# Performance work log

Measured on AMD Instinct MI355X. Metric: run time of the kernel, lower is better.

The kernel has to match this reference:

```python
import jax, jax.numpy as jnp
import numpy as np

B, T, N, F = 4, 24, 1024, 128
EPS = 1e-5  # torch nn.LayerNorm default
FRONT_T = 12  # hard-coded graph_array[:12] split in the original module
MIN_NUMBER = 3  # hard-coded topk k


def setup_inputs() -> dict:
    key = jax.random.key(0)
    ks = jax.random.split(key, 7)
    sc = 0.05
    return {
        "input": jax.random.normal(ks[0], (B, T, N, F), jnp.float32),
        # torch nn.Linear stores weight as [out, in]; y = x @ W.T + b
        "W_xff": jax.random.normal(ks[1], (3 * F, F), jnp.float32) * sc,
        "b_xff": jax.random.normal(ks[2], (3 * F,), jnp.float32) * sc,
        "W_ff1": jax.random.normal(ks[3], (F, F), jnp.float32) * sc,
        "b_ff1": jnp.zeros((F,), jnp.float32),
        "W_ff2": jax.random.normal(ks[4], (F, F), jnp.float32) * sc,
        "b_ff2": jnp.zeros((F,), jnp.float32),
        "ln_g": jnp.ones((F,), jnp.float32),
        "ln_b": jnp.zeros((F,), jnp.float32),
    }


def _mixup_last(front, y):
    # front: [12, N, F]; y: scalar int (data-dependent column index).
    # mixup_region with block_size=1: replace column y with the mean of
    # columns [max(y-1,0), min(y+2,N)), cast through uint8 (as original).
    n = front.shape[1]
    y_start = jnp.maximum(y - 1, 0)
    y_end = jnp.minimum(y + 2, n)
    cols = jnp.arange(n)
    mask = ((cols >= y_start) & (cols < y_end)).astype(front.dtype)  # [N]
    cnt = (y_end - y_start).astype(front.dtype)
    mixed = (front * mask[None, :, None]).sum(axis=1) / cnt  # [12, F]
    # .to(torch.uint8) truncates and kills gradient for this column
    mixed = jax.lax.stop_gradient(mixed.astype(jnp.uint8).astype(front.dtype))
    return front.at[:, y, :].set(mixed)


def reference(input, W_xff, b_xff, W_ff1, b_ff1, W_ff2, b_ff2, ln_g, ln_b):
    f = input.shape[-1]
    x_ = input @ W_xff.T + b_xff  # [B,T,N,3F]
    q, k, v = x_[..., :f], x_[..., f:2 * f], x_[..., 2 * f:]
    e = jnp.einsum('btnf,btmf->btnm', q, k) / jnp.sqrt(jnp.asarray(f, x_.dtype))
    attn = jax.nn.softmax(e, axis=-1)  # [B,T,N,N]

    # detached attention maps drive the topk row selection
    attn_d = jax.lax.stop_gradient(attn)
    col_sums = attn_d.sum(axis=2)  # torch sum(dim=1) per [T,N,N] -> [B,T,N]
    # torch.topk(largest=False, sorted=True): 3 smallest, ascending by value
    _, idx = jax.lax.top_k(-col_sums, MIN_NUMBER)  # [B,T,3]
    # NOTE: the original loop reassigns `graph_array = mixup_region(graph_array_front, ...)`
    # each iteration, so only the LAST mixup (i = T-1, 3rd smallest index) survives.
    y_last = idx[:, -1, -1]  # [B]

    front = v[:, :FRONT_T]   # [B,12,N,F]
    back = v[:, FRONT_T:]    # [B,T-12,N,F]
    new_front = jax.vmap(_mixup_last)(front, y_last)
    new_value = jnp.concatenate([new_front, back], axis=1)  # [B,T,N,F]

    value_i = jnp.einsum('btnm,btmf->btnf', attn, new_value)
    h = jax.nn.gelu(value_i @ W_ff1.T + b_ff1, approximate=False) @ W_ff2.T + b_ff2
    res = h + input
    mu = res.mean(-1, keepdims=True)
    var = ((res - mu) ** 2).mean(-1, keepdims=True)
    return (res - mu) / jnp.sqrt(var + EPS) * ln_g + ln_b
```

## Files before the change

kernel.cpp:

```cpp
#include <hip/hip_runtime.h>
#include <math.h>

#define BB 4
#define TT 24
#define BN 1024
#define FD 128
#define BT (BB*TT)
#define BTN (BT*BN)
#define FRONT_T 12
#define SCALE 0.08838834764831845f
#define GELU_K 0.7071067811865476f

typedef __attribute__((ext_vector_type(8))) short s8v;
typedef __attribute__((ext_vector_type(4))) float f4v;

static __device__ __forceinline__ unsigned short f2bf(float f) {
    union { float f; unsigned u; } c; c.f = f;
    unsigned u = c.u + 0x7FFFu + ((c.u >> 16) & 1u);
    return (unsigned short)(u >> 16);
}

__global__ __launch_bounds__(256) void k_convx(const float* __restrict__ x,
                                               unsigned short* __restrict__ xb) {
    size_t i = ((size_t)blockIdx.x * 256 + threadIdx.x) * 4;
    float4 v = *(const float4*)(x + i);
    ushort4 h = {f2bf(v.x), f2bf(v.y), f2bf(v.z), f2bf(v.w)};
    *(ushort4*)(xb + i) = h;
}

__global__ void k_convw(const float* __restrict__ W, unsigned short* __restrict__ wb, int n) {
    int i = blockIdx.x * 256 + threadIdx.x;
    if (i < n) wb[i] = f2bf(W[i]);
}

__global__ __launch_bounds__(256, 2) void k_qkv_mfma(
    const unsigned short* __restrict__ xb, const unsigned short* __restrict__ wb,
    const float* __restrict__ bias,
    unsigned short* __restrict__ qb16, unsigned short* __restrict__ kb16,
    unsigned short* __restrict__ vtb)
{
    __shared__ __attribute__((aligned(16))) unsigned short Xs[64 * 136];
    __shared__ __attribute__((aligned(16))) unsigned short Ws[64 * 136];
    __shared__ __attribute__((aligned(16))) unsigned short Cs[64 * 72];
    const int tid = threadIdx.x;
    const int rowBase = blockIdx.x * 64;
    const int colBase = blockIdx.y * 64;
    const int lane = tid & 63, wave = tid >> 6;
    const int lx = lane & 15, quad = lane >> 4;

    for (int i = 0; i < 4; ++i) {
        int idx = i * 256 + tid, r = idx >> 4, c8 = idx & 15;
        *(int4*)(&Xs[r * 136 + c8 * 8]) = *(const int4*)(xb + (size_t)(rowBase + r) * FD + c8 * 8);
    }
    for (int i = 0; i < 4; ++i) {
        int idx = i * 256 + tid, r = idx >> 4, c8 = idx & 15;
        *(int4*)(&Ws[r * 136 + c8 * 8]) = *(const int4*)(wb + (size_t)(colBase + r) * FD + c8 * 8);
    }
    __syncthreads();

    f4v acc[4];
    for (int gg = 0; gg < 4; ++gg) acc[gg] = (f4v){0.f, 0.f, 0.f, 0.f};
    for (int t4 = 0; t4 < 4; ++t4) {
        s8v a = *(const s8v*)(&Xs[(wave * 16 + lx) * 136 + t4 * 32 + quad * 8]);
        for (int gg = 0; gg < 4; ++gg) {
            s8v b = *(const s8v*)(&Ws[(gg * 16 + lx) * 136 + t4 * 32 + quad * 8]);
            acc[gg] = __builtin_amdgcn_mfma_f32_16x16x32_bf16(a, b, acc[gg], 0, 0, 0);
        }
    }

    const int n0 = wave * 16 + quad * 4;
    if (colBase < 2 * FD) {
        for (int gg = 0; gg < 4; ++gg) {
            float bb = bias[colBase + gg * 16 + lx];
            for (int r = 0; r < 4; ++r)
                Cs[(n0 + r) * 72 + gg * 16 + lx] = f2bf(acc[gg][r] + bb);
        }
        __syncthreads();
        unsigned short* dst = (colBase < FD) ? qb16 : kb16;
        const int cc0 = colBase & (FD - 1);
        for (int i = 0; i < 2; ++i) {
            int idx = i * 256 + tid, r = idx >> 3, c8 = idx & 7;
            *(int4*)(dst + (size_t)(rowBase + r) * FD + cc0 + c8 * 8) =
                *(const int4*)(&Cs[r * 72 + c8 * 8]);
        }
    } else {
        for (int gg = 0; gg < 4; ++gg) {
            float bb = bias[colBase + gg * 16 + lx];
            for (int r = 0; r < 4; ++r)
                Cs[(gg * 16 + lx) * 72 + n0 + r] = f2bf(acc[gg][r] + bb);
        }
        __syncthreads();
        const int bt = rowBase >> 10, nBase = rowBase & 1023, cc0 = colBase - 2 * FD;
        for (int i = 0; i < 2; ++i) {
            int idx = i * 256 + tid, f = idx >> 3, c8 = idx & 7;
            *(int4*)(vtb + ((size_t)bt * FD + cc0 + f) * BN + nBase + c8 * 8) =
                *(const int4*)(&Cs[f * 72 + c8 * 8]);
        }
    }
}

__global__ __launch_bounds__(256) void k_qkv32(const float* __restrict__ x,
                                               const float* __restrict__ W,
                                               const float* __restrict__ bias,
                                               float* __restrict__ q32c,
                                               float* __restrict__ k32c) {
    __shared__ float Xs[32][129];
    __shared__ float Ws[64][129];
    const int tid = threadIdx.x;
    const int b = blockIdx.x >> 5;
    const int rt = blockIdx.x & 31;
    const int xrow0 = (b * TT + (TT - 1)) * BN + rt * 32;
    const int colBase = blockIdx.y * 64;

    for (int i = 0; i < 4; ++i) {
        int idx = i * 256 + tid;
        int r = idx >> 5, c4 = idx & 31;
        *(float4*)(&Xs[r][c4 * 4]) = *(const float4*)(x + (size_t)(xrow0 + r) * FD + c4 * 4);
    }
    for (int i = 0; i < 8; ++i) {
        int idx = i * 256 + tid;
        int r = idx >> 5, c4 = idx & 31;
        *(float4*)(&Ws[r][c4 * 4]) = *(const float4*)(W + (size_t)(colBase + r) * FD + c4 * 4);
    }
    __syncthreads();

    const int tx = tid & 15, ty = tid >> 4;
    const int r0 = ty * 2, r1 = ty * 2 + 1;
    float acc0[4] = {0.f, 0.f, 0.f, 0.f};
    float acc1[4] = {0.f, 0.f, 0.f, 0.f};
    for (int kk = 0; kk < FD; ++kk) {
        float a0 = Xs[r0][kk], a1 = Xs[r1][kk];
        float b0 = Ws[tx * 4 + 0][kk];
        float b1 = Ws[tx * 4 + 1][kk];
        float b2 = Ws[tx * 4 + 2][kk];
        float b3 = Ws[tx * 4 + 3][kk];
        acc0[0] += a0 * b0; acc0[1] += a0 * b1; acc0[2] += a0 * b2; acc0[3] += a0 * b3;
        acc1[0] += a1 * b0; acc1[1] += a1 * b1; acc1[2] += a1 * b2; acc1[3] += a1 * b3;
    }
    const int c = colBase + tx * 4;
    float4 bia = *(const float4*)(bias + c);
    float* dst = (c < FD) ? q32c : k32c;
    int cc = (c < FD) ? c : c - FD;
    size_t base = ((size_t)b * BN + rt * 32 + r0) * FD + cc;
    *(float4*)(dst + base)      = make_float4(acc0[0] + bia.x, acc0[1] + bia.y, acc0[2] + bia.z, acc0[3] + bia.w);
    *(float4*)(dst + base + FD) = make_float4(acc1[0] + bia.x, acc1[1] + bia.y, acc1[2] + bia.z, acc1[3] + bia.w);
}

__global__ __launch_bounds__(256) void k_pass1(const float* __restrict__ q32c,
                                               const float* __restrict__ k32c,
                                               float* __restrict__ Mp,
                                               float* __restrict__ Lp) {
    __shared__ float Qs[32][129];
    __shared__ float Ks[64][129];
    const int tid = threadIdx.x;
    const int chunk = blockIdx.y;
    const int b = blockIdx.z;
    const int rowBase = blockIdx.x * 32;
    const float* qb = q32c + (size_t)b * BN * FD;
    const float* kb = k32c + (size_t)b * BN * FD;

    for (int i = 0; i < 4; ++i) {
        int idx = i * 256 + tid;
        int r = idx >> 5, c4 = idx & 31;
        *(float4*)(&Qs[r][c4 * 4]) = *(const float4*)(qb + (size_t)(rowBase + r) * FD + c4 * 4);
    }
    const int tx = tid & 15, ty = tid >> 4;
    const int r0 = ty * 2, r1 = ty * 2 + 1;
    float m[2] = {-1e30f, -1e30f};
    float l[2] = {0.f, 0.f};

    for (int ct = chunk * 4; ct < chunk * 4 + 4; ++ct) {
        __syncthreads();
        for (int i = 0; i < 8; ++i) {
            int idx = i * 256 + tid;
            int r = idx >> 5, c4 = idx & 31;
            *(float4*)(&Ks[r][c4 * 4]) = *(const float4*)(kb + (size_t)(ct * 64 + r) * FD + c4 * 4);
        }
        __syncthreads();
        float e0[4] = {0.f, 0.f, 0.f, 0.f};
        float e1[4] = {0.f, 0.f, 0.f, 0.f};
        for (int kk = 0; kk < FD; ++kk) {
            float a0 = Qs[r0][kk], a1 = Qs[r1][kk];
            float b0 = Ks[tx * 4 + 0][kk];
            float b1 = Ks[tx * 4 + 1][kk];
            float b2 = Ks[tx * 4 + 2][kk];
            float b3 = Ks[tx * 4 + 3][kk];
            e0[0] += a0 * b0; e0[1] += a0 * b1; e0[2] += a0 * b2; e0[3] += a0 * b3;
            e1[0] += a1 * b0; e1[1] += a1 * b1; e1[2] += a1 * b2; e1[3] += a1 * b3;
        }
        float* ep[2] = {e0, e1};
        for (int rr = 0; rr < 2; ++rr) {
            float s0 = ep[rr][0] * SCALE, s1 = ep[rr][1] * SCALE;
            float s2 = ep[rr][2] * SCALE, s3 = ep[rr][3] * SCALE;
            float tm = fmaxf(fmaxf(s0, s1), fmaxf(s2, s3));
            for (int s = 1; s < 16; s <<= 1) tm = fmaxf(tm, __shfl_xor(tm, s, 64));
            float ts = __expf(s0 - tm) + __expf(s1 - tm) + __expf(s2 - tm) + __expf(s3 - tm);
            for (int s = 1; s < 16; s <<= 1) ts += __shfl_xor(ts, s, 64);
            float mn = fmaxf(m[rr], tm);
            l[rr] = l[rr] * __expf(m[rr] - mn) + ts * __expf(tm - mn);
            m[rr] = mn;
        }
    }
    if (tx == 0) {
        size_t base = (size_t)chunk * BB * BN + (size_t)b * BN + rowBase;
        Mp[base + r0] = m[0];
        Lp[base + r0] = l[0];
        Mp[base + r1] = m[1];
        Lp[base + r1] = l[1];
    }
}

__global__ void k_mergeML(const float* __restrict__ Mp, const float* __restrict__ Lp,
                          float* __restrict__ Mv, float* __restrict__ Lv) {
    int i = blockIdx.x * 256 + threadIdx.x;
    if (i >= BB * BN) return;
    float m = -1e30f, l = 0.f;
    for (int c = 0; c < 4; ++c) {
        float mc = Mp[(size_t)c * BB * BN + i];
        float lc = Lp[(size_t)c * BB * BN + i];
        float mn = fmaxf(m, mc);
        l = l * __expf(m - mn) + lc * __expf(mc - mn);
        m = mn;
    }
    Mv[i] = m;
    Lv[i] = l;
}

__global__ __launch_bounds__(256) void k_colsum(const float* __restrict__ q32c,
                                                const float* __restrict__ k32c,
                                                const float* __restrict__ Mv,
                                                const float* __restrict__ Lv,
                                                float* __restrict__ csp) {
    __shared__ float Qs[32][129];
    __shared__ float Ks[64][129];
    __shared__ float red[16][68];
    const int tid = threadIdx.x;
    const int rchunk = blockIdx.y;
    const int b = blockIdx.z;
    const int colBase = blockIdx.x * 64;
    const float* qb = q32c + (size_t)b * BN * FD;
    const float* kb = k32c + (size_t)b * BN * FD;
    const int tx = tid & 15, ty = tid >> 4;
    const int r0 = ty * 2, r1 = ty * 2 + 1;

    for (int i = 0; i < 8; ++i) {
        int idx = i * 256 + tid;
        int r = idx >> 5, c4 = idx & 31;
        *(float4*)(&Ks[r][c4 * 4]) = *(const float4*)(kb + (size_t)(colBase + r) * FD + c4 * 4);
    }

    float acc[4] = {0.f, 0.f, 0.f, 0.f};
    for (int rt = rchunk * 4; rt < rchunk * 4 + 4; ++rt) {
        __syncthreads();
        for (int i = 0; i < 4; ++i) {
            int idx = i * 256 + tid;
            int r = idx >> 5, c4 = idx & 31;
            *(float4*)(&Qs[r][c4 * 4]) = *(const float4*)(qb + (size_t)(rt * 32 + r) * FD + c4 * 4);
        }
        __syncthreads();
        float e0[4] = {0.f, 0.f, 0.f, 0.f};
        float e1[4] = {0.f, 0.f, 0.f, 0.f};
        for (int kk = 0; kk < FD; ++kk) {
            float a0 = Qs[r0][kk], a1 = Qs[r1][kk];
            float b0 = Ks[tx * 4 + 0][kk];
            float b1 = Ks[tx * 4 + 1][kk];
            float b2 = Ks[tx * 4 + 2][kk];
            float b3 = Ks[tx * 4 + 3][kk];
            e0[0] += a0 * b0; e0[1] += a0 * b1; e0[2] += a0 * b2; e0[3] += a0 * b3;
            e1[0] += a1 * b0; e1[1] += a1 * b1; e1[2] += a1 * b2; e1[3] += a1 * b3;
        }
        int n0 = rt * 32 + r0, n1 = rt * 32 + r1;
        float m0 = Mv[(size_t)b * BN + n0], il0 = 1.0f / Lv[(size_t)b * BN + n0];
        float m1 = Mv[(size_t)b * BN + n1], il1 = 1.0f / Lv[(size_t)b * BN + n1];
        for (int j = 0; j < 4; ++j) {
            acc[j] += __expf(e0[j] * SCALE - m0) * il0;
            acc[j] += __expf(e1[j] * SCALE - m1) * il1;
        }
    }
    for (int j = 0; j < 4; ++j) red[ty][tx * 4 + j] = acc[j];
    __syncthreads();
    if (tid < 64) {
        float s = 0.f;
        for (int i = 0; i < 16; ++i) s += red[i][tid];
        csp[((size_t)rchunk * BB + b) * BN + colBase + tid] = s;
    }
}

__global__ void k_top3(const float* __restrict__ csp, int* __restrict__ ylast) {
    __shared__ float sv[192];
    __shared__ int si[192];
    const int b = blockIdx.x;
    const int t = threadIdx.x;
    float bv[3] = {1e30f, 1e30f, 1e30f};
    int bi[3] = {0x7fffffff, 0x7fffffff, 0x7fffffff};
    for (int i = 0; i < 16; ++i) {
        int idx = t * 16 + i;
        float vv = 0.f;
        for (int c = 0; c < 8; ++c)
            vv += csp[((size_t)c * BB + b) * BN + idx];
        if (vv < bv[0]) {
            bv[2] = bv[1]; bi[2] = bi[1];
            bv[1] = bv[0]; bi[1] = bi[0];
            bv[0] = vv;    bi[0] = idx;
        } else if (vv < bv[1]) {
            bv[2] = bv[1]; bi[2] = bi[1];
            bv[1] = vv;    bi[1] = idx;
        } else if (vv < bv[2]) {
            bv[2] = vv;    bi[2] = idx;
        }
    }
    for (int j = 0; j < 3; ++j) { sv[t * 3 + j] = bv[j]; si[t * 3 + j] = bi[j]; }
    __syncthreads();
    if (t == 0) {
        float fv[3] = {1e30f, 1e30f, 1e30f};
        int fi[3] = {0x7fffffff, 0x7fffffff, 0x7fffffff};
        for (int c = 0; c < 192; ++c) {
            float vv = sv[c]; int ii = si[c];
            if (vv < fv[0] || (vv == fv[0] && ii < fi[0])) {
                fv[2] = fv[1]; fi[2] = fi[1];
                fv[1] = fv[0]; fi[1] = fi[0];
                fv[0] = vv;    fi[0] = ii;
            } else if (vv < fv[1] || (vv == fv[1] && ii < fi[1])) {
                fv[2] = fv[1]; fi[2] = fi[1];
                fv[1] = vv;    fi[1] = ii;
            } else if (vv < fv[2] || (vv == fv[2] && ii < fi[2])) {
                fv[2] = vv;    fi[2] = ii;
            }
        }
        ylast[b] = fi[2];
    }
}

__global__ void k_mixup(const float* __restrict__ x, const float* __restrict__ W,
                        const float* __restrict__ bias,
                        unsigned short* __restrict__ vtb,
                        const int* __restrict__ ylast) {
    const int b = blockIdx.y, t = blockIdx.x, f = threadIdx.x;
    const int y = ylast[b];
    const int ys = max(y - 1, 0), ye = min(y + 2, BN);
    const float* wrow = W + (size_t)(2 * FD + f) * FD;
    const float bia = bias[2 * FD + f];
    float s = 0.f;
    for (int r = ys; r < ye; ++r) {
        const float* xrow = x + ((size_t)(b * TT + t) * BN + r) * FD;
        float acc = 0.f;
        for (int kk = 0; kk < FD; ++kk) acc += xrow[kk] * wrow[kk];
        s += acc + bia;
    }
    s /= (float)(ye - ys);
    int ti = (int)s;
    unsigned u = ((unsigned)ti) & 0xFFu;
    vtb[((size_t)(b * TT + t) * FD + f) * BN + y] = f2bf((float)u);
}

__global__ __launch_bounds__(256, 2) void k_flash(
    const unsigned short* __restrict__ qb, const unsigned short* __restrict__ kb,
    const unsigned short* __restrict__ vtb, float* __restrict__ vi)
{
    __shared__ __attribute__((aligned(16))) unsigned short Qs[64 * 136];
    __shared__ __attribute__((aligned(16))) unsigned short Ks[64 * 136];
    __shared__ __attribute__((aligned(16))) unsigned short Vts[128 * 72];
    __shared__ __attribute__((aligned(16))) unsigned short Ps[4][16 * 72];
    const int tid = threadIdx.x;
    const int bt = blockIdx.y;
    const int rowBase = blockIdx.x * 64;
    const int lane = tid & 63, wave = tid >> 6;
    const int lx = lane & 15, quad = lane >> 4;

    const unsigned short* qg = qb + ((size_t)bt * BN + rowBase) * FD;
    for (int i = 0; i < 4; ++i) {
        int idx = i * 256 + tid, r = idx >> 4, c8 = idx & 15;
        *(int4*)(&Qs[r * 136 + c8 * 8]) = *(const int4*)(qg + r * FD + c8 * 8);
    }
    __syncthreads();

    s8v aq[4];
    for (int t4 = 0; t4 < 4; ++t4)
        aq[t4] = *(const s8v*)(&Qs[(wave * 16 + lx) * 136 + t4 * 32 + quad * 8]);

    f4v O[8];
    for (int gg = 0; gg < 8; ++gg) O[gg] = (f4v){0.f, 0.f, 0.f, 0.f};
    float mrow[4] = {-1e30f, -1e30f, -1e30f, -1e30f};
    float lrow[4] = {0.f, 0.f, 0.f, 0.f};

    const unsigned short* kgbase = kb + (size_t)bt * BN * FD;
    const unsigned short* vgbase = vtb + (size_t)bt * FD * BN;

    for (int ct = 0; ct < 16; ++ct) {
        __syncthreads();
        const unsigned short* kg = kgbase + (size_t)ct * 64 * FD;
        for (int i = 0; i < 4; ++i) {
            int idx = i * 256 + tid, r = idx >> 4, c8 = idx & 15;
            *(int4*)(&Ks[r * 136 + c8 * 8]) = *(const int4*)(kg + r * FD + c8 * 8);
        }
        for (int i = 0; i < 4; ++i) {
            int idx = i * 256 + tid, r = idx >> 3, c8 = idx & 7;
            *(int4*)(&Vts[r * 72 + c8 * 8]) = *(const int4*)(vgbase + (size_t)r * BN + ct * 64 + c8 * 8);
        }
        __syncthreads();

        f4v e[4];
        for (int n4 = 0; n4 < 4; ++n4) {
            f4v acc = (f4v){0.f, 0.f, 0.f, 0.f};
            for (int t4 = 0; t4 < 4; ++t4) {
                s8v bk = *(const s8v*)(&Ks[(n4 * 16 + lx) * 136 + t4 * 32 + quad * 8]);
                acc = __builtin_amdgcn_mfma_f32_16x16x32_bf16(aq[t4], bk, acc, 0, 0, 0);
            }
            for (int r = 0; r < 4; ++r) acc[r] *= SCALE;
            e[n4] = acc;
        }
        for (int r = 0; r < 4; ++r) {
            float tm = fmaxf(fmaxf(e[0][r], e[1][r]), fmaxf(e[2][r], e[3][r]));
            for (int s = 1; s < 16; s <<= 1) tm = fmaxf(tm, __shfl_xor(tm, s, 64));
            float mn = fmaxf(mrow[r], tm);
            float alpha = __expf(mrow[r] - mn);
            mrow[r] = mn;
            float ps = 0.f;
            for (int n4 = 0; n4 < 4; ++n4) {
                float p = __expf(e[n4][r] - mn);
                e[n4][r] = p;
                ps += p;
            }
            for (int s = 1; s < 16; s <<= 1) ps += __shfl_xor(ps, s, 64);
            lrow[r] = lrow[r] * alpha + ps;
            for (int gg = 0; gg < 8; ++gg) O[gg][r] *= alpha;
        }
        for (int n4 = 0; n4 < 4; ++n4)
            for (int r = 0; r < 4; ++r)
                Ps[wave][(quad * 4 + r) * 72 + n4 * 16 + lx] = f2bf(e[n4][r]);
        for (int k2 = 0; k2 < 2; ++k2) {
            s8v ap = *(const s8v*)(&Ps[wave][lx * 72 + k2 * 32 + quad * 8]);
            for (int gg = 0; gg < 8; ++gg) {
                s8v bv = *(const s8v*)(&Vts[(gg * 16 + lx) * 72 + k2 * 32 + quad * 8]);
                O[gg] = __builtin_amdgcn_mfma_f32_16x16x32_bf16(ap, bv, O[gg], 0, 0, 0);
            }
        }
    }
    const int row0 = rowBase + wave * 16 + quad * 4;
    for (int r = 0; r < 4; ++r) {
        float inv = 1.0f / lrow[r];
        for (int gg = 0; gg < 8; ++gg)
            vi[((size_t)bt * BN + row0 + r) * FD + gg * 16 + lx] = O[gg][r] * inv;
    }
}

__global__ __launch_bounds__(256) void k_ffn(const float* __restrict__ vi,
                                             const float* __restrict__ x,
                                             const float* __restrict__ W1,
                                             const float* __restrict__ b1,
                                             const float* __restrict__ W2,
                                             const float* __restrict__ b2,
                                             const float* __restrict__ g,
                                             const float* __restrict__ lb,
                                             float* __restrict__ out) {
    __shared__ float Qs[32][132];
    __shared__ float KVs[64][132];
    const int tid = threadIdx.x;
    const int bt = blockIdx.y;
    const int rowBase = blockIdx.x * 32;
    const int tx = tid & 15, ty = tid >> 4;
    const int r0 = ty * 2, r1 = ty * 2 + 1;

    const float* vb = vi + ((size_t)bt * BN + rowBase) * FD;
    for (int i = 0; i < 4; ++i) {
        int idx = i * 256 + tid;
        int r = idx >> 5, c4 = idx & 31;
        *(float4*)(&Qs[r][c4 * 4]) = *(const float4*)(vb + (size_t)r * FD + c4 * 4);
    }

    float h0[8], h1[8];
    {
        float t0[8] = {}, t1[8] = {};
        for (int ch = 0; ch < 2; ++ch) {
            __syncthreads();
            for (int i = 0; i < 8; ++i) {
                int idx = i * 256 + tid;
                int r = idx >> 5, c4 = idx & 31;
                *(float4*)(&KVs[r][c4 * 4]) = *(const float4*)(W1 + (size_t)(ch * 64 + r) * FD + c4 * 4);
            }
            __syncthreads();
            for (int kk = 0; kk < FD; ++kk) {
                float u0 = Qs[r0][kk], u1 = Qs[r1][kk];
                for (int jj = 0; jj < 4; ++jj) {
                    int j = jj + 4 * ch;
                    float w = KVs[tx + 16 * jj][kk];
                    t0[j] += u0 * w;
                    t1[j] += u1 * w;
                }
            }
        }
        for (int j = 0; j < 8; ++j) {
            int f = tx + 16 * j;
            float bj = b1[f];
            float z0 = t0[j] + bj, z1 = t1[j] + bj;
            h0[j] = 0.5f * z0 * (1.0f + erff(z0 * GELU_K));
            h1[j] = 0.5f * z1 * (1.0f + erff(z1 * GELU_K));
        }
    }
    __syncthreads();
    for (int j = 0; j < 8; ++j) { Qs[r0][tx + 16 * j] = h0[j]; Qs[r1][tx + 16 * j] = h1[j]; }
    __syncthreads();

    float z0[8], z1[8];
    {
        float t0[8] = {}, t1[8] = {};
        for (int ch = 0; ch < 2; ++ch) {
            __syncthreads();
            for (int i = 0; i < 8; ++i) {
                int idx = i * 256 + tid;
                int r = idx >> 5, c4 = idx & 31;
                *(float4*)(&KVs[r][c4 * 4]) = *(const float4*)(W2 + (size_t)(ch * 64 + r) * FD + c4 * 4);
            }
            __syncthreads();
            for (int kk = 0; kk < FD; ++kk) {
                float u0 = Qs[r0][kk], u1 = Qs[r1][kk];
                for (int jj = 0; jj < 4; ++jj) {
                    int j = jj + 4 * ch;
                    float w = KVs[tx + 16 * jj][kk];
                    t0[j] += u0 * w;
                    t1[j] += u1 * w;
                }
            }
        }
        for (int j = 0; j < 8; ++j) {
            int f = tx + 16 * j;
            float bj = b2[f];
            z0[j] = t0[j] + bj;
            z1[j] = t1[j] + bj;
        }
    }

    const float* xb = x + ((size_t)bt * BN + rowBase) * FD;
    float res0[8], res1[8];
    float s0 = 0.f, s1 = 0.f;
    for (int j = 0; j < 8; ++j) {
        int f = tx + 16 * j;
        res0[j] = z0[j] + xb[(size_t)r0 * FD + f];
        res1[j] = z1[j] + xb[(size_t)r1 * FD + f];
        s0 += res0[j];
        s1 += res1[j];
    }
    for (int s = 1; s < 16; s <<= 1) { s0 += __shfl_xor(s0, s, 64); s1 += __shfl_xor(s1, s, 64); }
    const float mu0 = s0 * (1.0f / FD), mu1 = s1 * (1.0f / FD);
    float q0 = 0.f, q1 = 0.f;
    for (int j = 0; j < 8; ++j) {
        float d0 = res0[j] - mu0, d1 = res1[j] - mu1;
        q0 += d0 * d0;
        q1 += d1 * d1;
    }
    for (int s = 1; s < 16; s <<= 1) { q0 += __shfl_xor(q0, s, 64); q1 += __shfl_xor(q1, s, 64); }
    const float rs0 = rsqrtf(q0 * (1.0f / FD) + 1e-5f);
    const float rs1 = rsqrtf(q1 * (1.0f / FD) + 1e-5f);
    float* ob = out + ((size_t)bt * BN + rowBase) * FD;
    for (int j = 0; j < 8; ++j) {
        int f = tx + 16 * j;
        float gf = g[f], bf = lb[f];
        ob[(size_t)r0 * FD + f] = (res0[j] - mu0) * rs0 * gf + bf;
        ob[(size_t)r1 * FD + f] = (res1[j] - mu1) * rs1 * gf + bf;
    }
}

extern "C" void kernel_launch(void* const* d_in, const int* in_sizes, int n_in,
                              void* d_out, int out_size, void* d_ws, size_t ws_size,
                              hipStream_t stream) {
    const float* x     = (const float*)d_in[0];
    const float* W_xff = (const float*)d_in[1];
    const float* b_xff = (const float*)d_in[2];
    const float* W_ff1 = (const float*)d_in[3];
    const float* b_ff1 = (const float*)d_in[4];
    const float* W_ff2 = (const float*)d_in[5];
    const float* b_ff2 = (const float*)d_in[6];
    const float* ln_g  = (const float*)d_in[7];
    const float* ln_b  = (const float*)d_in[8];
    float* out = (float*)d_out;

    char* w = (char*)d_ws;
    unsigned short* qb16 = (unsigned short*)w;  w += (size_t)BTN * FD * 2;
    unsigned short* kb16 = (unsigned short*)w;  w += (size_t)BTN * FD * 2;
    unsigned short* vtb  = (unsigned short*)w;  w += (size_t)BTN * FD * 2;
    unsigned short* wxb  = (unsigned short*)w;  w += (size_t)3 * FD * FD * 2;
    char* alias = w;
    float* vi = (float*)alias;
    unsigned short* xb = (unsigned short*)alias; alias += (size_t)BTN * FD * 2;
    float* q32c = (float*)alias;                alias += (size_t)BB * BN * FD * 4;
    float* k32c = (float*)alias;                alias += (size_t)BB * BN * FD * 4;
    float* Mv   = (float*)alias;                alias += (size_t)BB * BN * 4;
    float* Lv   = (float*)alias;                alias += (size_t)BB * BN * 4;
    int* ylast  = (int*)alias;                  alias += 256;
    float* Mp   = (float*)alias;                alias += (size_t)4 * BB * BN * 4;
    float* Lp   = (float*)alias;                alias += (size_t)4 * BB * BN * 4;
    float* csp  = (float*)alias;                alias += (size_t)8 * BB * BN * 4;

    k_convx    <<<dim3(BTN * FD / 1024), 256, 0, stream>>>(x, xb);
    k_convw    <<<dim3(192),             256, 0, stream>>>(W_xff, wxb, 3 * FD * FD);
    k_qkv_mfma <<<dim3(BTN / 64, 6),     256, 0, stream>>>(xb, wxb, b_xff, qb16, kb16, vtb);
    k_qkv32    <<<dim3(BB * 32, 4),      256, 0, stream>>>(x, W_xff, b_xff, q32c, k32c);
    k_pass1    <<<dim3(32, 4, BB),       256, 0, stream>>>(q32c, k32c, Mp, Lp);
    k_mergeML  <<<dim3((BB * BN + 255) / 256), 256, 0, stream>>>(Mp, Lp, Mv, Lv);
    k_colsum   <<<dim3(16, 8, BB),       256, 0, stream>>>(q32c, k32c, Mv, Lv, csp);
    k_top3     <<<dim3(BB),               64, 0, stream>>>(csp, ylast);
    k_mixup    <<<dim3(FRONT_T, BB),     128, 0, stream>>>(x, W_xff, b_xff, vtb, ylast);
    k_flash    <<<dim3(16, BT),          256, 0, stream>>>(qb16, kb16, vtb, vi);
    k_ffn      <<<dim3(32, BT),          256, 0, stream>>>(vi, x, W_ff1, b_ff1, W_ff2, b_ff2,
                                                           ln_g, ln_b, out);
}
```

Measured before the change: 544.0 us.

## Process 128 query rows per flash block to reuse K/V tiles twice

The flash attention kernel now handles two 64-row query groups per block (128 rows), so each K and V tile loaded into shared memory serves twice as many rows, halving K/V global traffic. Q is loaded straight from global into registers, with no shared-memory stage. The grid is halved and block indices are remapped to interleave batch-time slices across blocks. Launch bounds ask for 3 blocks per SM. The doubled accumulator and register state raises register pressure, which may cause spills or limit occupancy.

Measured after the change: 531.9 us. 1.02x faster.

```diff
diff --git a/kernel.cpp b/kernel.cpp
--- a/kernel.cpp
+++ b/kernel.cpp
@@ -353,35 +353,35 @@
     vtb[((size_t)(b * TT + t) * FD + f) * BN + y] = f2bf((float)u);
 }
 
-__global__ __launch_bounds__(256, 2) void k_flash(
+__global__ __launch_bounds__(256, 3) void k_flash(
     const unsigned short* __restrict__ qb, const unsigned short* __restrict__ kb,
     const unsigned short* __restrict__ vtb, float* __restrict__ vi)
 {
-    __shared__ __attribute__((aligned(16))) unsigned short Qs[64 * 136];
     __shared__ __attribute__((aligned(16))) unsigned short Ks[64 * 136];
     __shared__ __attribute__((aligned(16))) unsigned short Vts[128 * 72];
     __shared__ __attribute__((aligned(16))) unsigned short Ps[4][16 * 72];
     const int tid = threadIdx.x;
-    const int bt = blockIdx.y;
-    const int rowBase = blockIdx.x * 64;
+    const int f = blockIdx.y * 8 + blockIdx.x;
+    const int s = (f & 7) * 96 + (f >> 3);
+    const int bt = s >> 3;
+    const int rowBase = (s & 7) * 128;
     const int lane = tid & 63, wave = tid >> 6;
     const int lx = lane & 15, quad = lane >> 4;
 
     const unsigned short* qg = qb + ((size_t)bt * BN + rowBase) * FD;
-    for (int i = 0; i < 4; ++i) {
-        int idx = i * 256 + tid, r = idx >> 4, c8 = idx & 15;
-        *(int4*)(&Qs[r * 136 + c8 * 8]) = *(const int4*)(qg + r * FD + c8 * 8);
-    }
-    __syncthreads();
-
-    s8v aq[4];
-    for (int t4 = 0; t4 < 4; ++t4)
-        aq[t4] = *(const s8v*)(&Qs[(wave * 16 + lx) * 136 + t4 * 32 + quad * 8]);
-
-    f4v O[8];
-    for (int gg = 0; gg < 8; ++gg) O[gg] = (f4v){0.f, 0.f, 0.f, 0.f};
-    float mrow[4] = {-1e30f, -1e30f, -1e30f, -1e30f};
-    float lrow[4] = {0.f, 0.f, 0.f, 0.f};
+    s8v aq[2][4];
+    #pragma unroll
+    for (int rg = 0; rg < 2; ++rg)
+        #pragma unroll
+        for (int t4 = 0; t4 < 4; ++t4)
+            aq[rg][t4] = *(const s8v*)(qg + (size_t)(rg * 64 + wave * 16 + lx) * FD + t4 * 32 + quad * 8);
+
+    f4v O[2][8];
+    #pragma unroll
+    for (int rg = 0; rg < 2; ++rg)
+        for (int gg = 0; gg < 8; ++gg) O[rg][gg] = (f4v){0.f, 0.f, 0.f, 0.f};
+    float mrow[2][4] = {{-1e30f, -1e30f, -1e30f, -1e30f}, {-1e30f, -1e30f, -1e30f, -1e30f}};
+    float lrow[2][4] = {{0.f, 0.f, 0.f, 0.f}, {0.f, 0.f, 0.f, 0.f}};
 
     const unsigned short* kgbase = kb + (size_t)bt * BN * FD;
     const unsigned short* vgbase = vtb + (size_t)bt * FD * BN;
@@ -399,48 +399,54 @@
         }
         __syncthreads();
 
-        f4v e[4];
-        for (int n4 = 0; n4 < 4; ++n4) {
-            f4v acc = (f4v){0.f, 0.f, 0.f, 0.f};
-            for (int t4 = 0; t4 < 4; ++t4) {
-                s8v bk = *(const s8v*)(&Ks[(n4 * 16 + lx) * 136 + t4 * 32 + quad * 8]);
-                acc = __builtin_amdgcn_mfma_f32_16x16x32_bf16(aq[t4], bk, acc, 0, 0, 0);
-            }
-            for (int r = 0; r < 4; ++r) acc[r] *= SCALE;
-            e[n4] = acc;
-        }
+        #pragma unroll
+        for (int rg = 0; rg < 2; ++rg) {
+            f4v e[4];
+            for (int n4 = 0; n4 < 4; ++n4) {
+                f4v acc = (f4v){0.f, 0.f, 0.f, 0.f};
+                for (int t4 = 0; t4 < 4; ++t4) {
+                    s8v bk = *(const s8v*)(&Ks[(n4 * 16 + lx) * 136 + t4 * 32 + quad * 8]);
+                    acc = __builtin_amdgcn_mfma_f32_16x16x32_bf16(aq[rg][t4], bk, acc, 0, 0, 0);
+                }
+                for (int r = 0; r < 4; ++r) acc[r] *= SCALE;
+                e[n4] = acc;
+            }
+            for (int r = 0; r < 4; ++r) {
+                float tm = fmaxf(fmaxf(e[0][r], e[1][r]), fmaxf(e[2][r], e[3][r]));
+                for (int s2 = 1; s2 < 16; s2 <<= 1) tm = fmaxf(tm, __shfl_xor(tm, s2, 64));
+                float mn = fmaxf(mrow[rg][r], tm);
+                float alpha = __expf(mrow[rg][r] - mn);
+                mrow[rg][r] = mn;
+                float ps = 0.f;
+                for (int n4 = 0; n4 < 4; ++n4) {
+                    float p = __expf(e[n4][r] - mn);
+                    e[n4][r] = p;
+                    ps += p;
+                }
+                for (int s2 = 1; s2 < 16; s2 <<= 1) ps += __shfl_xor(ps, s2, 64);
+                lrow[rg][r] = lrow[rg][r] * alpha + ps;
+                for (int gg = 0; gg < 8; ++gg) O[rg][gg][r] *= alpha;
+            }
+            for (int n4 = 0; n4 < 4; ++n4)
+                for (int r = 0; r < 4; ++r)
+                    Ps[wave][(quad * 4 + r) * 72 + n4 * 16 + lx] = f2bf(e[n4][r]);
+            for (int k2 = 0; k2 < 2; ++k2) {
+                s8v ap = *(const s8v*)(&Ps[wave][lx * 72 + k2 * 32 + quad * 8]);
+                for (int gg = 0; gg < 8; ++gg) {
+                    s8v bv = *(const s8v*)(&Vts[(gg * 16 + lx) * 72 + k2 * 32 + quad * 8]);
+                    O[rg][gg] = __builtin_amdgcn_mfma_f32_16x16x32_bf16(ap, bv, O[rg][gg], 0, 0, 0);
+                }
+            }
+        }
+    }
+    #pragma unroll
+    for (int rg = 0; rg < 2; ++rg) {
+        const int row0 = rowBase + rg * 64 + wave * 16 + quad * 4;
         for (int r = 0; r < 4; ++r) {
-            float tm = fmaxf(fmaxf(e[0][r], e[1][r]), fmaxf(e[2][r], e[3][r]));
-            for (int s = 1; s < 16; s <<= 1) tm = fmaxf(tm, __shfl_xor(tm, s, 64));
-            float mn = fmaxf(mrow[r], tm);
-            float alpha = __expf(mrow[r] - mn);
-            mrow[r] = mn;
-            float ps = 0.f;
-            for (int n4 = 0; n4 < 4; ++n4) {
-                float p = __expf(e[n4][r] - mn);
-                e[n4][r] = p;
-                ps += p;
-            }
-            for (int s = 1; s < 16; s <<= 1) ps += __shfl_xor(ps, s, 64);
-            lrow[r] = lrow[r] * alpha + ps;
-            for (int gg = 0; gg < 8; ++gg) O[gg][r] *= alpha;
-        }
-        for (int n4 = 0; n4 < 4; ++n4)
-            for (int r = 0; r < 4; ++r)
-                Ps[wave][(quad * 4 + r) * 72 + n4 * 16 + lx] = f2bf(e[n4][r]);
-        for (int k2 = 0; k2 < 2; ++k2) {
-            s8v ap = *(const s8v*)(&Ps[wave][lx * 72 + k2 * 32 + quad * 8]);
-            for (int gg = 0; gg < 8; ++gg) {
-                s8v bv = *(const s8v*)(&Vts[(gg * 16 + lx) * 72 + k2 * 32 + quad * 8]);
-                O[gg] = __builtin_amdgcn_mfma_f32_16x16x32_bf16(ap, bv, O[gg], 0, 0, 0);
-            }
-        }
-    }
-    const int row0 = rowBase + wave * 16 + quad * 4;
-    for (int r = 0; r < 4; ++r) {
-        float inv = 1.0f / lrow[r];
-        for (int gg = 0; gg < 8; ++gg)
-            vi[((size_t)bt * BN + row0 + r) * FD + gg * 16 + lx] = O[gg][r] * inv;
+            float inv = 1.0f / lrow[rg][r];
+            for (int gg = 0; gg < 8; ++gg)
+                vi[((size_t)bt * BN + row0 + r) * FD + gg * 16 + lx] = O[rg][gg][r] * inv;
+        }
     }
 }
 
@@ -600,7 +606,7 @@
     k_colsum   <<<dim3(16, 8, BB),       256, 0, stream>>>(q32c, k32c, Mv, Lv, csp);
     k_top3     <<<dim3(BB),               64, 0, stream>>>(csp, ylast);
     k_mixup    <<<dim3(FRONT_T, BB),     128, 0, stream>>>(x, W_xff, b_xff, vtb, ylast);
-    k_flash    <<<dim3(16, BT),          256, 0, stream>>>(qb16, kb16, vtb, vi);
+    k_flash    <<<dim3(8, BT),           256, 0, stream>>>(qb16, kb16, vtb, vi);
     k_ffn      <<<dim3(32, BT),          256, 0, stream>>>(vi, x, W_ff1, b_ff1, W_ff2, b_ff2,
                                                            ln_g, ln_b, out);
 }
```
